# Kernel tuning notes

Hardware: AMD Instinct MI355X
Metric: run time of the kernel (lower is better)

## Reference

```python
import jax, jax.numpy as jnp
import numpy as np
import itertools, math

M_MODES = 10
N_PHOT = 5
IN_MODES = np.array([0, 2, 4, 6, 8])  # input_state = [1,0,1,0,...], 5 photons
INV_SQRT2 = 0.7071067811865476

# Fock output bases (lexicographic ordering)
ROWS_NB = np.array(list(itertools.combinations(range(M_MODES), N_PHOT)), np.int32)          # [252,5] no-bunching
ROWS_B = np.array(list(itertools.combinations_with_replacement(range(M_MODES), N_PHOT)), np.int32)  # [2002,5] bunched

def _norms(rows):
    out = []
    for r in rows:
        c = np.bincount(r, minlength=M_MODES)
        out.append(float(np.prod([math.factorial(int(v)) for v in c])))
    return np.array(out, np.float32)

NORM_NB = _norms(ROWS_NB)  # all ones
NORM_B = _norms(ROWS_B)

# Glynn sign vectors for n=5 permanents (delta_0 fixed to +1): [16,5]
_D = np.array(list(itertools.product([1.0, -1.0], repeat=N_PHOT - 1)), np.float32)
DELTAS = np.concatenate([np.ones((_D.shape[0], 1), np.float32), _D], axis=1)
DSIGNS = np.prod(DELTAS, axis=1)


def _mzi(t1, t2):
    # BS // PS(t1) // BS // PS(t2); BS = (1/sqrt2)[[1,i],[i,1]], PS on first mode of pair
    B = jnp.array([[1.0, 1.0j], [1.0j, 1.0]], dtype=jnp.complex64) * INV_SQRT2
    e1 = jnp.exp(1j * t1)
    e2 = jnp.exp(1j * t2)
    M1 = B * jnp.stack([e1, jnp.ones_like(e1)])[:, None]   # PS(t1) @ BS
    M2 = B @ M1                                            # BS @ ...
    return M2 * jnp.stack([e2, jnp.ones_like(e2)])[:, None]  # PS(t2) @ ...


def interferometer(phases):
    """Rectangular (Clements) mesh on 10 modes with 45 MZIs; phases [45,2] -> U [10,10] complex."""
    Ts = jax.vmap(lambda p: _mzi(p[0], p[1]))(phases)  # [45,2,2]
    U = jnp.eye(M_MODES, dtype=jnp.complex64)
    k = 0
    for layer in range(M_MODES):
        for p in range(layer % 2, M_MODES - 1, 2):
            U = U.at[p:p + 2, :].set(Ts[k] @ U[p:p + 2, :])
            k += 1
    return U


def batched_permanent(Ms):
    """Glynn formula for [...,5,5] complex matrices."""
    D = jnp.asarray(DELTAS, dtype=Ms.dtype)       # [16,5]
    s = jnp.asarray(DSIGNS, dtype=Ms.dtype)       # [16]
    rowsum = jnp.einsum('di,...ij->...dj', D, Ms)  # [...,16,5]
    return jnp.einsum('d,...d->...', s, jnp.prod(rowsum, axis=-1)) / (2 ** (N_PHOT - 1))


def fock_probs(U, rows, norm):
    """U [B,10,10]; rows [K,5] output-mode indices (with repetition for bunching); norm [K]."""
    M = U[:, rows][..., IN_MODES]        # [B,K,5,5]
    perm = batched_permanent(M)          # [B,K]
    return (jnp.abs(perm) ** 2) / jnp.asarray(norm)


def _forward(x, W_down, b_down, phases_l1, phases_r1, phases_lf, phases_rf, W_out, b_out):
    h = (x @ W_down + b_down) / jnp.pi                 # downscale + DivideByPi -> [B,10]
    WL1 = interferometer(phases_l1)
    WR1 = interferometer(phases_r1)
    U1 = jnp.einsum('mk,bk,kn->bmn', WR1, jnp.exp(1j * h), WL1)  # WR @ diag(e^{i phi}) @ WL
    e1 = fock_probs(U1, ROWS_NB, NORM_NB)              # [B,252], no_bunching=True
    # final circuit: 252 px phase shifters round-robin over 10 modes -> phases add per mode
    Bsz = e1.shape[0]
    pad = jnp.pad(e1, ((0, 0), (0, 260 - 252)))
    phi2 = pad.reshape(Bsz, 26, M_MODES).sum(axis=1)   # [B,10]
    WLF = interferometer(phases_lf)
    WRF = interferometer(phases_rf)
    UF = jnp.einsum('mk,bk,kn->bmn', WRF, jnp.exp(1j * phi2), WLF)
    probs = fock_probs(UF, ROWS_B, NORM_B)             # [B,2002], bunched Fock states
    return probs @ W_out + b_out                       # [B,num_classes]


def setup_inputs() -> dict:
    key = jax.random.key(0)
    ks = jax.random.split(key, 9)
    two_pi = 2.0 * np.pi
    return {
        'x': jax.random.normal(ks[0], (128, 784), dtype=jnp.float32),
        'W_down': jax.random.normal(ks[1], (784, 10), dtype=jnp.float32) * 0.05,
        'b_down': jax.random.normal(ks[2], (10,), dtype=jnp.float32) * 0.05,
        'phases_l1': jax.random.uniform(ks[3], (45, 2), dtype=jnp.float32) * two_pi,
        'phases_r1': jax.random.uniform(ks[4], (45, 2), dtype=jnp.float32) * two_pi,
        'phases_lf': jax.random.uniform(ks[5], (45, 2), dtype=jnp.float32) * two_pi,
        'phases_rf': jax.random.uniform(ks[6], (45, 2), dtype=jnp.float32) * two_pi,
        'W_out': jax.random.normal(ks[7], (2002, 10), dtype=jnp.float32) * 0.02,
        'b_out': jax.random.normal(ks[8], (10,), dtype=jnp.float32) * 0.02,
    }


def reference(x, W_down, b_down, phases_l1, phases_r1, phases_lf, phases_rf, W_out, b_out):
    return _forward(x, W_down, b_down, phases_l1, phases_r1, phases_lf, phases_rf, W_out, b_out)
```

## Files before the change

### kernel.cpp

```cpp
#include <hip/hip_runtime.h>
#include <math.h>


#define PI_F 3.14159265358979323846f

__constant__ float FACTF[6] = {1.f, 1.f, 2.f, 6.f, 24.f, 120.f};

__device__ __forceinline__ float2 cmul(float2 a, float2 b) {
  return make_float2(fmaf(a.x, b.x, -a.y * b.y), fmaf(a.x, b.y, a.y * b.x));
}
__device__ __forceinline__ float2 cadd(float2 a, float2 b) {
  return make_float2(a.x + b.x, a.y + b.y);
}
__device__ __forceinline__ float2 cscale(float2 a, float s) {
  return make_float2(a.x * s, a.y * s);
}
__device__ __forceinline__ float2 imul(float2 a) {
  return make_float2(-a.y, a.x);
}

__device__ __forceinline__ void unrank5f(int rank, float cnt0, float m0,
                                         int c[5]) {
  float r = (float)rank;
  float cnt = cnt0, m = m0, j = 4.f;
  int x = 0;
#pragma unroll
  for (int i = 0; i < 5; i++) {
    while (r >= cnt) {
      r -= cnt;
      cnt = cnt * (m - j) / m;
      m -= 1.f;
      x++;
    }
    c[i] = x;
    cnt = cnt * j / m;
    m -= 1.f;
    j -= 1.f;
    x++;
  }
}

__device__ __forceinline__ float2 prod5(const float2 rs[5]) {
  return cmul(cmul(cmul(rs[0], rs[1]), cmul(rs[2], rs[3])), rs[4]);
}

__device__ __forceinline__ float2 perm5(const float2 M[5][5]) {
  float2 rs[5];
#pragma unroll
  for (int j = 0; j < 5; j++) {
    rs[j] = M[0][j];
#pragma unroll
    for (int i = 1; i < 5; i++) rs[j] = cadd(rs[j], M[i][j]);
  }
  float2 acc = prod5(rs);
#pragma unroll
  for (int t = 1; t < 16; t++) {
    const int g = t ^ (t >> 1);
    const int bit = (t & 1) ? 0 : ((t & 2) ? 1 : ((t & 4) ? 2 : 3));
    const int i = bit + 1;
    const float step = ((g >> bit) & 1) ? -2.0f : 2.0f;
#pragma unroll
    for (int j = 0; j < 5; j++) {
      rs[j].x = fmaf(step, M[i][j].x, rs[j].x);
      rs[j].y = fmaf(step, M[i][j].y, rs[j].y);
    }
    float2 p = prod5(rs);
    const float s = (__popc(g) & 1) ? -1.0f : 1.0f;
    acc.x = fmaf(s, p.x, acc.x);
    acc.y = fmaf(s, p.y, acc.y);
  }
  return make_float2(acc.x * (1.0f / 16.0f), acc.y * (1.0f / 16.0f));
}

__global__ __launch_bounds__(256) void k_prefix(
    const float* __restrict__ x, const float* __restrict__ Wd,
    const float* __restrict__ bd, const float* __restrict__ ph_l1,
    const float* __restrict__ ph_r1, const float* __restrict__ ph_lf,
    const float* __restrict__ ph_rf, const float* __restrict__ bout,
    float2* __restrict__ UFws, float* __restrict__ out) {
  const int b = blockIdx.x, tid = threadIdx.x;

  __shared__ float2 T[4][45][4];
  __shared__ float2 Ui[4][100];
  __shared__ float2 A[100];
  __shared__ float2 Ub[100];
  __shared__ float  e1s[252];
  __shared__ float  red[4][10];
  __shared__ float2 v[10];

  float hacc[10];
#pragma unroll
  for (int c = 0; c < 10; c++) hacc[c] = 0.f;
  for (int i = tid; i < 784; i += 256) {
    float xv = x[b * 784 + i];
    const float* w = Wd + i * 10;
#pragma unroll
    for (int c = 0; c < 10; c++) hacc[c] = fmaf(xv, w[c], hacc[c]);
  }

  if (tid < 180) {
    const int which = tid / 45, m = tid % 45;
    const float* ph = (which == 0) ? ph_l1
                    : (which == 1) ? ph_r1
                    : (which == 2) ? ph_lf : ph_rf;
    float t1 = ph[m * 2 + 0], t2 = ph[m * 2 + 1];
    float s1, c1, s2, c2;
    sincosf(t1, &s1, &c1);
    sincosf(t2, &s2, &c2);
    float2 e2  = make_float2(c2, s2);
    float2 e1m = make_float2(c1 - 1.f, s1);
    float2 e1p = make_float2(c1 + 1.f, s1);
    T[which][m][0] = cscale(cmul(e2, e1m), 0.5f);
    T[which][m][1] = cscale(cmul(e2, imul(e1p)), 0.5f);
    T[which][m][2] = cscale(imul(e1p), 0.5f);
    T[which][m][3] = make_float2(0.5f * (1.f - c1), -0.5f * s1);
  }
  for (int idx = tid; idx < 400; idx += 256)
    Ui[idx / 100][idx % 100] =
        make_float2((idx % 100) % 11 == 0 ? 1.f : 0.f, 0.f);

  {
    const int lane = tid & 63, wave = tid >> 6;
#pragma unroll
    for (int c = 0; c < 10; c++) {
      float r = hacc[c];
#pragma unroll
      for (int d = 32; d > 0; d >>= 1) r += __shfl_down(r, d);
      if (lane == 0) red[wave][c] = r;
    }
  }

  int kb = 0;
  for (int layer = 0; layer < 10; layer++) {
    __syncthreads();
    const int start = layer & 1;
    const int npairs = 5 - start;
    if (tid < 200) {
      const int which = tid / 50, tl = tid % 50;
      if (tl < npairs * 10) {
        const int pi = tl / 10, n = tl % 10;
        const int p = start + 2 * pi;
        const int k = kb + pi;
        float2 u0 = Ui[which][p * 10 + n], u1 = Ui[which][(p + 1) * 10 + n];
        float2 n0 = cadd(cmul(T[which][k][0], u0), cmul(T[which][k][1], u1));
        float2 n1 = cadd(cmul(T[which][k][2], u0), cmul(T[which][k][3], u1));
        Ui[which][p * 10 + n] = n0;
        Ui[which][(p + 1) * 10 + n] = n1;
      }
    }
    kb += npairs;
  }
  __syncthreads();

  if (tid < 10) {
    float s = red[0][tid] + red[1][tid] + red[2][tid] + red[3][tid] + bd[tid];
    s *= (1.0f / PI_F);
    float sn, cs;
    sincosf(s, &sn, &cs);
    v[tid] = make_float2(cs, sn);
  }
  __syncthreads();

  if (tid < 100) A[tid] = cmul(Ui[1][tid], v[tid % 10]);
  __syncthreads();
  if (tid < 100) {
    const int m = tid / 10, n = tid % 10;
    float2 acc = make_float2(0.f, 0.f);
#pragma unroll
    for (int k = 0; k < 10; k++)
      acc = cadd(acc, cmul(A[m * 10 + k], Ui[0][k * 10 + n]));
    Ub[tid] = acc;
  }
  __syncthreads();

  if (tid < 252) {
    int c[5];
    unrank5f(tid, 126.f, 9.f, c);
    float2 M[5][5];
#pragma unroll
    for (int i = 0; i < 5; i++)
#pragma unroll
      for (int j = 0; j < 5; j++) M[i][j] = Ub[c[i] * 10 + 2 * j];
    float2 p = perm5(M);
    e1s[tid] = p.x * p.x + p.y * p.y;
  }
  __syncthreads();

  if (tid < 10) {
    float s = 0.f;
    for (int idx = tid; idx < 252; idx += 10) s += e1s[idx];
    float sn, cs;
    sincosf(s, &sn, &cs);
    v[tid] = make_float2(cs, sn);
  }
  __syncthreads();

  if (tid < 100) A[tid] = cmul(Ui[3][tid], v[tid % 10]);
  __syncthreads();
  if (tid < 100) {
    const int m = tid / 10, n = tid % 10;
    float2 acc = make_float2(0.f, 0.f);
#pragma unroll
    for (int k = 0; k < 10; k++)
      acc = cadd(acc, cmul(A[m * 10 + k], Ui[2][k * 10 + n]));
    UFws[b * 100 + tid] = acc;
  }
  if (tid < 10) out[b * 10 + tid] = bout[tid];
}

__global__ __launch_bounds__(256) void k_perms(const float2* __restrict__ UFws,
                                               const float* __restrict__ Wout,
                                               float* __restrict__ out) {
  const int b = blockIdx.x >> 3, chunk = blockIdx.x & 7;
  const int tid = threadIdx.x;
  const int k = chunk * 256 + tid;
  __shared__ float2 U[100];
  __shared__ float red[4][10];
  if (tid < 100) U[tid] = UFws[b * 100 + tid];
  __syncthreads();

  float acc[10];
#pragma unroll
  for (int c = 0; c < 10; c++) acc[c] = 0.f;

  if (k < 2002) {
    int c5[5];
    unrank5f(k, 715.f, 13.f, c5);
    int modes[5];
#pragma unroll
    for (int i = 0; i < 5; i++) modes[i] = c5[i] - i;
    float2 M[5][5];
#pragma unroll
    for (int i = 0; i < 5; i++)
#pragma unroll
      for (int j = 0; j < 5; j++) M[i][j] = U[modes[i] * 10 + 2 * j];
    float2 p = perm5(M);
    float norm = 1.f;
    int run = 1;
#pragma unroll
    for (int i = 1; i < 5; i++) {
      if (modes[i] == modes[i - 1]) run++;
      else { norm *= FACTF[run]; run = 1; }
    }
    norm *= FACTF[run];
    const float pv = (p.x * p.x + p.y * p.y) / norm;
    const float2* w2 = (const float2*)Wout + k * 5;
#pragma unroll
    for (int c = 0; c < 5; c++) {
      float2 w = w2[c];
      acc[2 * c + 0] = pv * w.x;
      acc[2 * c + 1] = pv * w.y;
    }
  }

  const int lane = tid & 63, wave = tid >> 6;
#pragma unroll
  for (int c = 0; c < 10; c++) {
    float r = acc[c];
#pragma unroll
    for (int d = 32; d > 0; d >>= 1) r += __shfl_down(r, d);
    if (lane == 0) red[wave][c] = r;
  }
  __syncthreads();
  if (tid < 10) {
    float s = red[0][tid] + red[1][tid] + red[2][tid] + red[3][tid];
    atomicAdd(&out[b * 10 + tid], s);
  }
}

extern "C" void kernel_launch(void* const* d_in, const int* in_sizes, int n_in,
                              void* d_out, int out_size, void* d_ws,
                              size_t ws_size, hipStream_t stream) {
  const float* x    = (const float*)d_in[0];
  const float* Wd   = (const float*)d_in[1];
  const float* bd   = (const float*)d_in[2];
  const float* pl1  = (const float*)d_in[3];
  const float* pr1  = (const float*)d_in[4];
  const float* plf  = (const float*)d_in[5];
  const float* prf  = (const float*)d_in[6];
  const float* Wout = (const float*)d_in[7];
  const float* bout = (const float*)d_in[8];
  float* out = (float*)d_out;

  float2* UFws = (float2*)d_ws;

  k_prefix<<<128, 256, 0, stream>>>(x, Wd, bd, pl1, pr1, plf, prf, bout, UFws,
                                    out);
  k_perms<<<1024, 256, 0, stream>>>(UFws, Wout, out);
}
```

Measured before the change: 92.80 us.

## Fuse prefix and permanent kernels, recomputing per-sample prefix in every chunk block

Merges the two kernels into one launch of 1024 blocks. Each of the 8 chunk blocks per sample now recomputes the downsampling, interferometer, and 252 first-layer permanents instead of passing the final unitary through workspace. The Clements mesh is now built per column in registers by 40 threads, replacing ten barrier-separated shared-memory steps. The phase-scaling copy into A is folded into the matrix product. This removes a kernel boundary and several barriers, but adds an 8x redundant prefix computation plus a memset launch.

```diff
diff --git a/kernel.cpp b/kernel.cpp
--- a/kernel.cpp
+++ b/kernel.cpp
@@ -72,17 +72,17 @@
   return make_float2(acc.x * (1.0f / 16.0f), acc.y * (1.0f / 16.0f));
 }
 
-__global__ __launch_bounds__(256) void k_prefix(
+__global__ __launch_bounds__(256) void k_all(
     const float* __restrict__ x, const float* __restrict__ Wd,
     const float* __restrict__ bd, const float* __restrict__ ph_l1,
     const float* __restrict__ ph_r1, const float* __restrict__ ph_lf,
-    const float* __restrict__ ph_rf, const float* __restrict__ bout,
-    float2* __restrict__ UFws, float* __restrict__ out) {
-  const int b = blockIdx.x, tid = threadIdx.x;
+    const float* __restrict__ ph_rf, const float* __restrict__ Wout,
+    const float* __restrict__ bout, float* __restrict__ out) {
+  const int b = blockIdx.x >> 3, chunk = blockIdx.x & 7;
+  const int tid = threadIdx.x;
 
   __shared__ float2 T[4][45][4];
   __shared__ float2 Ui[4][100];
-  __shared__ float2 A[100];
   __shared__ float2 Ub[100];
   __shared__ float  e1s[252];
   __shared__ float  red[4][10];
@@ -115,9 +115,6 @@
     T[which][m][2] = cscale(imul(e1p), 0.5f);
     T[which][m][3] = make_float2(0.5f * (1.f - c1), -0.5f * s1);
   }
-  for (int idx = tid; idx < 400; idx += 256)
-    Ui[idx / 100][idx % 100] =
-        make_float2((idx % 100) % 11 == 0 ? 1.f : 0.f, 0.f);
 
   {
     const int lane = tid & 63, wave = tid >> 6;
@@ -129,46 +126,46 @@
       if (lane == 0) red[wave][c] = r;
     }
   }
-
-  int kb = 0;
-  for (int layer = 0; layer < 10; layer++) {
-    __syncthreads();
-    const int start = layer & 1;
-    const int npairs = 5 - start;
-    if (tid < 200) {
-      const int which = tid / 50, tl = tid % 50;
-      if (tl < npairs * 10) {
-        const int pi = tl / 10, n = tl % 10;
+  __syncthreads();
+
+  if (tid < 40) {
+    const int which = tid / 10, n = tid % 10;
+    float2 u[10];
+#pragma unroll
+    for (int m = 0; m < 10; m++)
+      u[m] = make_float2(m == n ? 1.f : 0.f, 0.f);
+    int kb = 0;
+#pragma unroll
+    for (int layer = 0; layer < 10; layer++) {
+      const int start = layer & 1;
+      const int npairs = 5 - start;
+      for (int pi = 0; pi < npairs; pi++) {
         const int p = start + 2 * pi;
         const int k = kb + pi;
-        float2 u0 = Ui[which][p * 10 + n], u1 = Ui[which][(p + 1) * 10 + n];
-        float2 n0 = cadd(cmul(T[which][k][0], u0), cmul(T[which][k][1], u1));
-        float2 n1 = cadd(cmul(T[which][k][2], u0), cmul(T[which][k][3], u1));
-        Ui[which][p * 10 + n] = n0;
-        Ui[which][(p + 1) * 10 + n] = n1;
+        float2 u0 = u[p], u1 = u[p + 1];
+        u[p]     = cadd(cmul(T[which][k][0], u0), cmul(T[which][k][1], u1));
+        u[p + 1] = cadd(cmul(T[which][k][2], u0), cmul(T[which][k][3], u1));
       }
-    }
-    kb += npairs;
-  }
-  __syncthreads();
-
-  if (tid < 10) {
-    float s = red[0][tid] + red[1][tid] + red[2][tid] + red[3][tid] + bd[tid];
+      kb += npairs;
+    }
+#pragma unroll
+    for (int m = 0; m < 10; m++) Ui[which][m * 10 + n] = u[m];
+  } else if (tid >= 64 && tid < 74) {
+    const int c = tid - 64;
+    float s = red[0][c] + red[1][c] + red[2][c] + red[3][c] + bd[c];
     s *= (1.0f / PI_F);
     float sn, cs;
     sincosf(s, &sn, &cs);
-    v[tid] = make_float2(cs, sn);
-  }
-  __syncthreads();
-
-  if (tid < 100) A[tid] = cmul(Ui[1][tid], v[tid % 10]);
-  __syncthreads();
+    v[c] = make_float2(cs, sn);
+  }
+  __syncthreads();
+
   if (tid < 100) {
     const int m = tid / 10, n = tid % 10;
     float2 acc = make_float2(0.f, 0.f);
 #pragma unroll
     for (int k = 0; k < 10; k++)
-      acc = cadd(acc, cmul(A[m * 10 + k], Ui[0][k * 10 + n]));
+      acc = cadd(acc, cmul(cmul(Ui[1][m * 10 + k], v[k]), Ui[0][k * 10 + n]));
     Ub[tid] = acc;
   }
   __syncthreads();
@@ -195,34 +192,20 @@
   }
   __syncthreads();
 
-  if (tid < 100) A[tid] = cmul(Ui[3][tid], v[tid % 10]);
-  __syncthreads();
   if (tid < 100) {
     const int m = tid / 10, n = tid % 10;
     float2 acc = make_float2(0.f, 0.f);
 #pragma unroll
     for (int k = 0; k < 10; k++)
-      acc = cadd(acc, cmul(A[m * 10 + k], Ui[2][k * 10 + n]));
-    UFws[b * 100 + tid] = acc;
-  }
-  if (tid < 10) out[b * 10 + tid] = bout[tid];
-}
-
-__global__ __launch_bounds__(256) void k_perms(const float2* __restrict__ UFws,
-                                               const float* __restrict__ Wout,
-                                               float* __restrict__ out) {
-  const int b = blockIdx.x >> 3, chunk = blockIdx.x & 7;
-  const int tid = threadIdx.x;
+      acc = cadd(acc, cmul(cmul(Ui[3][m * 10 + k], v[k]), Ui[2][k * 10 + n]));
+    Ub[tid] = acc;
+  }
+  __syncthreads();
+
+  float acc[10];
+#pragma unroll
+  for (int c = 0; c < 10; c++) acc[c] = 0.f;
   const int k = chunk * 256 + tid;
-  __shared__ float2 U[100];
-  __shared__ float red[4][10];
-  if (tid < 100) U[tid] = UFws[b * 100 + tid];
-  __syncthreads();
-
-  float acc[10];
-#pragma unroll
-  for (int c = 0; c < 10; c++) acc[c] = 0.f;
-
   if (k < 2002) {
     int c5[5];
     unrank5f(k, 715.f, 13.f, c5);
@@ -233,7 +216,7 @@
 #pragma unroll
     for (int i = 0; i < 5; i++)
 #pragma unroll
-      for (int j = 0; j < 5; j++) M[i][j] = U[modes[i] * 10 + 2 * j];
+      for (int j = 0; j < 5; j++) M[i][j] = Ub[modes[i] * 10 + 2 * j];
     float2 p = perm5(M);
     float norm = 1.f;
     int run = 1;
@@ -253,17 +236,20 @@
     }
   }
 
-  const int lane = tid & 63, wave = tid >> 6;
-#pragma unroll
-  for (int c = 0; c < 10; c++) {
-    float r = acc[c];
-#pragma unroll
-    for (int d = 32; d > 0; d >>= 1) r += __shfl_down(r, d);
-    if (lane == 0) red[wave][c] = r;
+  {
+    const int lane = tid & 63, wave = tid >> 6;
+#pragma unroll
+    for (int c = 0; c < 10; c++) {
+      float r = acc[c];
+#pragma unroll
+      for (int d = 32; d > 0; d >>= 1) r += __shfl_down(r, d);
+      if (lane == 0) red[wave][c] = r;
+    }
   }
   __syncthreads();
   if (tid < 10) {
     float s = red[0][tid] + red[1][tid] + red[2][tid] + red[3][tid];
+    if (chunk == 0) s += bout[tid];
     atomicAdd(&out[b * 10 + tid], s);
   }
 }
@@ -282,9 +268,7 @@
   const float* bout = (const float*)d_in[8];
   float* out = (float*)d_out;
 
-  float2* UFws = (float2*)d_ws;
-
-  k_prefix<<<128, 256, 0, stream>>>(x, Wd, bd, pl1, pr1, plf, prf, bout, UFws,
-                                    out);
-  k_perms<<<1024, 256, 0, stream>>>(UFws, Wout, out);
-}
+  hipMemsetAsync(out, 0, (size_t)out_size * sizeof(float), stream);
+  k_all<<<1024, 256, 0, stream>>>(x, Wd, bd, pl1, pr1, plf, prf, Wout, bout,
+                                  out);
+}
```

New measurement: 101.7 us. 1.1x slower.
